# Kernel optimization log

Hardware: AMD Instinct MI355X
Metric: run time of the kernel (lower is better)

The kernel has to match this reference:

```python
import jax, jax.numpy as jnp
import numpy as np

B, N, M, K = 8, 9225, 4096, 32
D = 2          # coordinate dim
HID = 64       # MLP hidden
DOUT = 16      # MLP output / f_y channels


def setup_inputs() -> dict:
    key = jax.random.key(0)
    ks = jax.random.split(key, 10)
    y = jax.random.uniform(ks[0], (B, N, D), dtype=jnp.float32)
    x = jax.random.uniform(ks[1], (B, M, D), dtype=jnp.float32)
    f_y = jax.random.uniform(ks[2], (B, N, DOUT), dtype=jnp.float32)
    weights = jax.random.uniform(ks[3], (B, N), dtype=jnp.float32)
    neighbors_index = jax.random.randint(ks[4], (B, M, K), 0, N, dtype=jnp.int64)
    drop = jax.random.uniform(ks[5], (B, M, K)) < 0.1
    neighbors_index = jnp.where(drop, jnp.int64(-1), neighbors_index)
    # LinearChannelMLP params: 4 -> 64 -> 16, gelu between
    W1 = jax.random.normal(ks[6], (2 * D, HID), dtype=jnp.float32) * (1.0 / np.sqrt(2 * D))
    b1 = jnp.zeros((HID,), dtype=jnp.float32)
    W2 = jax.random.normal(ks[7], (HID, DOUT), dtype=jnp.float32) * (1.0 / np.sqrt(HID))
    b2 = jnp.zeros((DOUT,), dtype=jnp.float32)
    return {"y": y, "x": x, "f_y": f_y, "weights": weights,
            "W1": W1, "b1": b1, "W2": W2, "b2": b2,
            "neighbors_index": neighbors_index}


def _batched_gather(table, idx):
    # table: [B, N, ...], idx: [B, M, K] -> [B, M, K, ...]
    return jax.vmap(lambda t, i: t[i])(table, idx)


def reference(y, x, f_y, weights, W1, b1, W2, b2, neighbors_index):
    idx = jnp.where(neighbors_index == -1, 0, neighbors_index)      # [B,M,K]
    valid = (neighbors_index != -1).astype(y.dtype)[..., None]      # [B,M,K,1]

    rep_y = _batched_gather(y, idx)                                 # [B,M,K,D]
    in_f = _batched_gather(f_y, idx)                                # [B,M,K,DOUT]
    self_x = jnp.broadcast_to(x[:, :, None, :], rep_y.shape)        # [B,M,K,D]

    agg = jnp.concatenate([rep_y, self_x], axis=-1)                 # [B,M,K,2D]
    h = jax.nn.gelu(agg @ W1 + b1, approximate=False)               # [B,M,K,HID]
    kval = h @ W2 + b2                                              # [B,M,K,DOUT]

    kval = kval * in_f                                              # linear transform: k(x,y)*f(y)
    w_nbr = _batched_gather(weights, idx)[..., None]                # [B,M,K,1]
    kval = kval * w_nbr * valid
    return kval.sum(axis=2)                                         # [B,M,DOUT]
```

## Files before the change

### kernel.cpp

```cpp
#include <hip/hip_runtime.h>
#include <hip/hip_bf16.h>

#define B_    8
#define N_    9225
#define M_    4096
#define K_    32
#define HID_  64
#define DOUT_ 16
#define SENT  (B_ * N_)

typedef __attribute__((ext_vector_type(8))) short short8;
typedef __attribute__((ext_vector_type(4))) float floatx4;
typedef __attribute__((ext_vector_type(2))) float f32x2;

static __device__ __forceinline__ short f2bf(float f) {
    __hip_bfloat16 h = __float2bfloat16(f);
    return __builtin_bit_cast(short, h);
}
static __device__ __forceinline__ unsigned pack2bf(float a, float b) {
    const unsigned lo = (unsigned)(unsigned short)__builtin_bit_cast(short, __float2bfloat16(a));
    const unsigned hi = (unsigned)(unsigned short)__builtin_bit_cast(short, __float2bfloat16(b));
    return (hi << 16) | lo;
}
static __device__ __forceinline__ f32x2 splat2(float v) { return (f32x2){v, v}; }
static __device__ __forceinline__ int bpermi(int src_bytes, int v) {
    return __builtin_amdgcn_ds_bpermute(src_bytes, v);
}

static __device__ __forceinline__ float row16_sum(float v) {
    int t;
    t = __builtin_amdgcn_update_dpp(0, __builtin_bit_cast(int, v), 0x111, 0xF, 0xF, true);
    v += __builtin_bit_cast(float, t);
    t = __builtin_amdgcn_update_dpp(0, __builtin_bit_cast(int, v), 0x112, 0xF, 0xF, true);
    v += __builtin_bit_cast(float, t);
    t = __builtin_amdgcn_update_dpp(0, __builtin_bit_cast(int, v), 0x114, 0xF, 0xF, true);
    v += __builtin_bit_cast(float, t);
    t = __builtin_amdgcn_update_dpp(0, __builtin_bit_cast(int, v), 0x118, 0xF, 0xF, true);
    v += __builtin_bit_cast(float, t);
    return v;
}

static __device__ __forceinline__ f32x2 gelu2(f32x2 x) {
    const f32x2 xsq = x * x;
    const f32x2 t   = __builtin_elementwise_fma(xsq, splat2(0.035677408f), splat2(0.79788456f));
    const f32x2 z   = x * t;
    const f32x2 u   = z * z;
    const f32x2 a   = u + splat2(105.0f);
    const f32x2 nin = __builtin_elementwise_fma(u, a, splat2(945.0f));
    const f32x2 num = z * nin;
    const f32x2 bq  = __builtin_elementwise_fma(u, splat2(15.0f), splat2(420.0f));
    const f32x2 den = __builtin_elementwise_fma(u, bq, splat2(945.0f));
    const f32x2 r   = { __builtin_amdgcn_rcpf(den[0]), __builtin_amdgcn_rcpf(den[1]) };
    f32x2 th = num * r;
    th = __builtin_elementwise_min(__builtin_elementwise_max(th, splat2(-1.0f)), splat2(1.0f));
    const f32x2 hx = x * splat2(0.5f);
    return __builtin_elementwise_fma(hx, th, hx);
}

__global__ __launch_bounds__(256) void prep_kernel(
    const float* __restrict__ y,
    const float* __restrict__ f_y,
    const float* __restrict__ w,
    unsigned*    __restrict__ pack)
{
    const int t = blockIdx.x * 256 + threadIdx.x;
    const int n = t >> 2, c = t & 3;
    if (n > SENT) return;
    uint4 o = {0u, 0u, 0u, 0u};
    if (n < SENT) {
        const floatx4 f = *(const floatx4*)(f_y + (size_t)n * 16 + c * 4);
        o.x = pack2bf(f[0], f[1]);
        o.y = pack2bf(f[2], f[3]);
        const float2 yv = *(const float2*)(y + (size_t)n * 2);
        o.z = pack2bf(yv.x, yv.y);
        o.w = __builtin_bit_cast(unsigned, w[n]);
    }
    *(uint4*)(pack + (size_t)n * 16 + c * 4) = o;
}

__global__ __launch_bounds__(256) void it_kernel(
    const float*    __restrict__ x,
    const float*    __restrict__ W1,
    const float*    __restrict__ b1,
    const float*    __restrict__ W2,
    const float*    __restrict__ b2,
    const int*      __restrict__ nbr,
    const unsigned* __restrict__ pack,
    float*          __restrict__ out)
{
    const int tid  = threadIdx.x;
    const int lane = tid & 63;
    const int q    = lane >> 4;
    const int nlo  = lane & 15;
    const int blk   = blockIdx.x;
    const int batch = blk & 7;
    const int pidx  = (blk >> 3) * 4 + (tid >> 6);
    const int row0  = __builtin_amdgcn_readfirstlane(batch * M_ + pidx * 2);
    const int bbase = batch * N_;

    const int r_g = lane >> 5, kk = lane & 31;
    const int raw = nbr[(size_t)(row0 + r_g) * K_ + kk];
    const int bn_g = (raw >= 0) ? (bbase + raw) : SENT;

    short8 a1f[4];
    #pragma unroll
    for (int t = 0; t < 4; ++t) {
        #pragma unroll
        for (int jj = 0; jj < 8; ++jj) {
            const int k = q * 8 + jj;
            float v = 0.0f;
            if (k < 4)       v = W1[k * 64 + t * 16 + nlo];
            else if (k == 4) v = b1[t * 16 + nlo];
            a1f[t][jj] = f2bf(v);
        }
    }

    short8 w2f[2];
    #pragma unroll
    for (int ch = 0; ch < 2; ++ch)
        #pragma unroll
        for (int jj = 0; jj < 8; ++jj) {
            const int j = (ch * 2 + (jj >> 2)) * 16 + q * 4 + (jj & 3);
            w2f[ch][jj] = f2bf(W2[j * DOUT_ + nlo]);
        }

    const floatx4 b2v = *(const floatx4*)(b2 + q * 4);
    const short one_bf = f2bf(1.0f);

    const float2 xv0 = *(const float2*)(x + (size_t)row0 * 2);
    const float2 xv1 = *(const float2*)(x + (size_t)row0 * 2 + 2);
    const short xb[2][2] = { { f2bf(xv0.x), f2bf(xv0.y) },
                             { f2bf(xv1.x), f2bf(xv1.y) } };

    float partial[4] = {0.f, 0.f, 0.f, 0.f};
    #pragma unroll
    for (int ph = 0; ph < 4; ++ph) {
        const int it = ph >> 1, h = ph & 1;
        const int src = ((it << 5) + (h << 4) + nlo) << 2;

        const int bn = bpermi(src, bn_g);
        const uint4 rec = *(const uint4*)(pack + (size_t)bn * 16 + q * 4);

        const float fv0 = __builtin_bit_cast(float, rec.x << 16);
        const float fv1 = __builtin_bit_cast(float, rec.x & 0xffff0000u);
        const float fv2 = __builtin_bit_cast(float, rec.y << 16);
        const float fv3 = __builtin_bit_cast(float, rec.y & 0xffff0000u);
        const float s   = __builtin_bit_cast(float, rec.w);

        short8 bfrag = {0, 0, 0, 0, 0, 0, 0, 0};
        if (q == 0) {
            bfrag[0] = (short)(rec.z & 0xffffu);
            bfrag[1] = (short)(rec.z >> 16);
            bfrag[2] = xb[it][0];
            bfrag[3] = xb[it][1];
            bfrag[4] = one_bf;
        }

        floatx4 accT[4];
        #pragma unroll
        for (int t = 0; t < 4; ++t) {
            floatx4 z4 = {0.f, 0.f, 0.f, 0.f};
            accT[t] = __builtin_amdgcn_mfma_f32_16x16x32_bf16(a1f[t], bfrag, z4, 0, 0, 0);
        }

        short8 hf[2];
        #pragma unroll
        for (int ch = 0; ch < 2; ++ch)
            #pragma unroll
            for (int half = 0; half < 2; ++half) {
                const floatx4 a = accT[ch * 2 + half];
                const f32x2 g0 = gelu2((f32x2){a[0], a[1]});
                const f32x2 g1 = gelu2((f32x2){a[2], a[3]});
                hf[ch][half * 4 + 0] = f2bf(g0[0]);
                hf[ch][half * 4 + 1] = f2bf(g0[1]);
                hf[ch][half * 4 + 2] = f2bf(g1[0]);
                hf[ch][half * 4 + 3] = f2bf(g1[1]);
            }

        floatx4 acc = b2v;
        acc = __builtin_amdgcn_mfma_f32_16x16x32_bf16(w2f[0], hf[0], acc, 0, 0, 0);
        acc = __builtin_amdgcn_mfma_f32_16x16x32_bf16(w2f[1], hf[1], acc, 0, 0, 0);
        partial[0] = fmaf(acc[0], fv0 * s, partial[0]);
        partial[1] = fmaf(acc[1], fv1 * s, partial[1]);
        partial[2] = fmaf(acc[2], fv2 * s, partial[2]);
        partial[3] = fmaf(acc[3], fv3 * s, partial[3]);

        if (h == 1) {
            #pragma unroll
            for (int r4 = 0; r4 < 4; ++r4)
                partial[r4] = row16_sum(partial[r4]);
            if (nlo == 15) {
                floatx4 o = {partial[0], partial[1], partial[2], partial[3]};
                *(floatx4*)(out + (size_t)(row0 + it) * DOUT_ + q * 4) = o;
            }
            #pragma unroll
            for (int r4 = 0; r4 < 4; ++r4) partial[r4] = 0.f;
        }
    }
}

extern "C" void kernel_launch(void* const* d_in, const int* in_sizes, int n_in,
                              void* d_out, int out_size, void* d_ws, size_t ws_size,
                              hipStream_t stream) {
    const float* y   = (const float*)d_in[0];
    const float* x   = (const float*)d_in[1];
    const float* f_y = (const float*)d_in[2];
    const float* w   = (const float*)d_in[3];
    const float* W1  = (const float*)d_in[4];
    const float* b1  = (const float*)d_in[5];
    const float* W2  = (const float*)d_in[6];
    const float* b2  = (const float*)d_in[7];
    const int*   nbr = (const int*)d_in[8];
    float* out = (float*)d_out;
    unsigned* pack = (unsigned*)d_ws;

    const int nthread = (SENT + 1) * 4;
    dim3 pgrid((nthread + 255) / 256), pblock(256);
    hipLaunchKernelGGL(prep_kernel, pgrid, pblock, 0, stream, y, f_y, w, pack);

    dim3 grid(B_ * M_ / 8), block(256);
    hipLaunchKernelGGL(it_kernel, grid, block, 0, stream,
                       x, W1, b1, W2, b2, nbr, pack, out);
}
```

Measured before the change: 110.9 us.

## Persistent loop over row pairs with prefetched indices and bias folded into MFMA accumulator

The grid shrinks from 4096 blocks to 1024, and each wave now loops over four row-pairs spaced 1024 apart. While computing the current pair it prefetches the next pair's neighbor indices and x coordinates, and it issues all four gathered record loads up front. b1 now initializes the first MFMA accumulator instead of riding a ones-row in the bf16 fragment, which keeps the bias in fp32. This amortizes weight-fragment setup across more work and overlaps gather latency, at the cost of more registers and fewer waves in flight.

```diff
diff --git a/kernel.cpp b/kernel.cpp
--- a/kernel.cpp
+++ b/kernel.cpp
@@ -94,26 +94,18 @@
     const int nlo  = lane & 15;
     const int blk   = blockIdx.x;
     const int batch = blk & 7;
-    const int pidx  = (blk >> 3) * 4 + (tid >> 6);
-    const int row0  = __builtin_amdgcn_readfirstlane(batch * M_ + pidx * 2);
+    const int pidx0 = (blk >> 3) * 4 + (tid >> 6);
     const int bbase = batch * N_;
-
-    const int r_g = lane >> 5, kk = lane & 31;
-    const int raw = nbr[(size_t)(row0 + r_g) * K_ + kk];
-    const int bn_g = (raw >= 0) ? (bbase + raw) : SENT;
+    const int r_g   = lane >> 5, kk = lane & 31;
 
     short8 a1f[4];
     #pragma unroll
-    for (int t = 0; t < 4; ++t) {
+    for (int t = 0; t < 4; ++t)
         #pragma unroll
         for (int jj = 0; jj < 8; ++jj) {
             const int k = q * 8 + jj;
-            float v = 0.0f;
-            if (k < 4)       v = W1[k * 64 + t * 16 + nlo];
-            else if (k == 4) v = b1[t * 16 + nlo];
-            a1f[t][jj] = f2bf(v);
-        }
-    }
+            a1f[t][jj] = f2bf(k < 4 ? W1[k * 64 + t * 16 + nlo] : 0.0f);
+        }
 
     short8 w2f[2];
     #pragma unroll
@@ -124,78 +116,98 @@
             w2f[ch][jj] = f2bf(W2[j * DOUT_ + nlo]);
         }
 
+    floatx4 b1v[4];
+    #pragma unroll
+    for (int t = 0; t < 4; ++t)
+        b1v[t] = *(const floatx4*)(b1 + t * 16 + q * 4);
     const floatx4 b2v = *(const floatx4*)(b2 + q * 4);
-    const short one_bf = f2bf(1.0f);
-
-    const float2 xv0 = *(const float2*)(x + (size_t)row0 * 2);
-    const float2 xv1 = *(const float2*)(x + (size_t)row0 * 2 + 2);
-    const short xb[2][2] = { { f2bf(xv0.x), f2bf(xv0.y) },
-                             { f2bf(xv1.x), f2bf(xv1.y) } };
-
-    float partial[4] = {0.f, 0.f, 0.f, 0.f};
-    #pragma unroll
-    for (int ph = 0; ph < 4; ++ph) {
-        const int it = ph >> 1, h = ph & 1;
-        const int src = ((it << 5) + (h << 4) + nlo) << 2;
-
-        const int bn = bpermi(src, bn_g);
-        const uint4 rec = *(const uint4*)(pack + (size_t)bn * 16 + q * 4);
-
-        const float fv0 = __builtin_bit_cast(float, rec.x << 16);
-        const float fv1 = __builtin_bit_cast(float, rec.x & 0xffff0000u);
-        const float fv2 = __builtin_bit_cast(float, rec.y << 16);
-        const float fv3 = __builtin_bit_cast(float, rec.y & 0xffff0000u);
-        const float s   = __builtin_bit_cast(float, rec.w);
-
-        short8 bfrag = {0, 0, 0, 0, 0, 0, 0, 0};
-        if (q == 0) {
-            bfrag[0] = (short)(rec.z & 0xffffu);
-            bfrag[1] = (short)(rec.z >> 16);
-            bfrag[2] = xb[it][0];
-            bfrag[3] = xb[it][1];
-            bfrag[4] = one_bf;
-        }
-
-        floatx4 accT[4];
-        #pragma unroll
-        for (int t = 0; t < 4; ++t) {
-            floatx4 z4 = {0.f, 0.f, 0.f, 0.f};
-            accT[t] = __builtin_amdgcn_mfma_f32_16x16x32_bf16(a1f[t], bfrag, z4, 0, 0, 0);
-        }
-
-        short8 hf[2];
-        #pragma unroll
-        for (int ch = 0; ch < 2; ++ch)
+
+    int row0 = __builtin_amdgcn_readfirstlane(batch * M_ + pidx0 * 2);
+    int raw  = nbr[(size_t)(row0 + r_g) * K_ + kk];
+    floatx4 xv = *(const floatx4*)(x + (size_t)row0 * 2);
+
+    #pragma unroll 1
+    for (int g = 0; g < 4; ++g) {
+        const int bn_g = (raw >= 0) ? (bbase + raw) : SENT;
+        uint4 rec[4];
+        #pragma unroll
+        for (int ph = 0; ph < 4; ++ph) {
+            const int srcl = ((ph >> 1) << 5) + ((ph & 1) << 4) + nlo;
+            const int bn = bpermi(srcl << 2, bn_g);
+            rec[ph] = *(const uint4*)(pack + (size_t)bn * 16 + q * 4);
+        }
+
+        const int rown = row0 + 1024;
+        int raw_n = 0; floatx4 xv_n = {0.f, 0.f, 0.f, 0.f};
+        if (g < 3) {
+            raw_n = nbr[(size_t)(rown + r_g) * K_ + kk];
+            xv_n  = *(const floatx4*)(x + (size_t)rown * 2);
+        }
+
+        const short xb[2][2] = { { f2bf(xv[0]), f2bf(xv[1]) },
+                                 { f2bf(xv[2]), f2bf(xv[3]) } };
+
+        float partial[4] = {0.f, 0.f, 0.f, 0.f};
+        #pragma unroll
+        for (int ph = 0; ph < 4; ++ph) {
+            const int it = ph >> 1, h = ph & 1;
+            const uint4 rc = rec[ph];
+
+            const float fv0 = __builtin_bit_cast(float, rc.x << 16);
+            const float fv1 = __builtin_bit_cast(float, rc.x & 0xffff0000u);
+            const float fv2 = __builtin_bit_cast(float, rc.y << 16);
+            const float fv3 = __builtin_bit_cast(float, rc.y & 0xffff0000u);
+            const float s   = __builtin_bit_cast(float, rc.w);
+
+            short8 bfrag = {0, 0, 0, 0, 0, 0, 0, 0};
+            if (q == 0) {
+                bfrag[0] = (short)(rc.z & 0xffffu);
+                bfrag[1] = (short)(rc.z >> 16);
+                bfrag[2] = xb[it][0];
+                bfrag[3] = xb[it][1];
+            }
+
+            floatx4 accT[4];
             #pragma unroll
-            for (int half = 0; half < 2; ++half) {
-                const floatx4 a = accT[ch * 2 + half];
-                const f32x2 g0 = gelu2((f32x2){a[0], a[1]});
-                const f32x2 g1 = gelu2((f32x2){a[2], a[3]});
-                hf[ch][half * 4 + 0] = f2bf(g0[0]);
-                hf[ch][half * 4 + 1] = f2bf(g0[1]);
-                hf[ch][half * 4 + 2] = f2bf(g1[0]);
-                hf[ch][half * 4 + 3] = f2bf(g1[1]);
+            for (int t = 0; t < 4; ++t)
+                accT[t] = __builtin_amdgcn_mfma_f32_16x16x32_bf16(a1f[t], bfrag, b1v[t], 0, 0, 0);
+
+            short8 hf[2];
+            #pragma unroll
+            for (int ch = 0; ch < 2; ++ch)
+                #pragma unroll
+                for (int half = 0; half < 2; ++half) {
+                    const floatx4 a = accT[ch * 2 + half];
+                    const f32x2 g0 = gelu2((f32x2){a[0], a[1]});
+                    const f32x2 g1 = gelu2((f32x2){a[2], a[3]});
+                    hf[ch][half * 4 + 0] = f2bf(g0[0]);
+                    hf[ch][half * 4 + 1] = f2bf(g0[1]);
+                    hf[ch][half * 4 + 2] = f2bf(g1[0]);
+                    hf[ch][half * 4 + 3] = f2bf(g1[1]);
+                }
+
+            floatx4 acc = b2v;
+            acc = __builtin_amdgcn_mfma_f32_16x16x32_bf16(w2f[0], hf[0], acc, 0, 0, 0);
+            acc = __builtin_amdgcn_mfma_f32_16x16x32_bf16(w2f[1], hf[1], acc, 0, 0, 0);
+            partial[0] = fmaf(acc[0], fv0 * s, partial[0]);
+            partial[1] = fmaf(acc[1], fv1 * s, partial[1]);
+            partial[2] = fmaf(acc[2], fv2 * s, partial[2]);
+            partial[3] = fmaf(acc[3], fv3 * s, partial[3]);
+
+            if (h == 1) {
+                #pragma unroll
+                for (int r4 = 0; r4 < 4; ++r4)
+                    partial[r4] = row16_sum(partial[r4]);
+                if (nlo == 15) {
+                    floatx4 o = {partial[0], partial[1], partial[2], partial[3]};
+                    *(floatx4*)(out + (size_t)(row0 + it) * DOUT_ + q * 4) = o;
+                }
+                #pragma unroll
+                for (int r4 = 0; r4 < 4; ++r4) partial[r4] = 0.f;
             }
-
-        floatx4 acc = b2v;
-        acc = __builtin_amdgcn_mfma_f32_16x16x32_bf16(w2f[0], hf[0], acc, 0, 0, 0);
-        acc = __builtin_amdgcn_mfma_f32_16x16x32_bf16(w2f[1], hf[1], acc, 0, 0, 0);
-        partial[0] = fmaf(acc[0], fv0 * s, partial[0]);
-        partial[1] = fmaf(acc[1], fv1 * s, partial[1]);
-        partial[2] = fmaf(acc[2], fv2 * s, partial[2]);
-        partial[3] = fmaf(acc[3], fv3 * s, partial[3]);
-
-        if (h == 1) {
-            #pragma unroll
-            for (int r4 = 0; r4 < 4; ++r4)
-                partial[r4] = row16_sum(partial[r4]);
-            if (nlo == 15) {
-                floatx4 o = {partial[0], partial[1], partial[2], partial[3]};
-                *(floatx4*)(out + (size_t)(row0 + it) * DOUT_ + q * 4) = o;
-            }
-            #pragma unroll
-            for (int r4 = 0; r4 < 4; ++r4) partial[r4] = 0.f;
-        }
+        }
+
+        row0 = rown; raw = raw_n; xv = xv_n;
     }
 }
 
@@ -218,7 +230,7 @@
     dim3 pgrid((nthread + 255) / 256), pblock(256);
     hipLaunchKernelGGL(prep_kernel, pgrid, pblock, 0, stream, y, f_y, w, pack);
 
-    dim3 grid(B_ * M_ / 8), block(256);
+    dim3 grid(1024), block(256);
     hipLaunchKernelGGL(it_kernel, grid, block, 0, stream,
                        x, W1, b1, W2, b2, nbr, pack, out);
 }
```

Result: no change. 110.9 us (+0.1%).
